# Performance work log

Hardware: AMD Instinct MI355X
Metric: run time of the kernel (lower is better)

The kernel has to match this reference:

```python
import jax, jax.numpy as jnp
import numpy as np

GROUP = 16  # FP4 quantization group size along the K (channel) axis
FP4_MAX = 6.0  # max magnitude representable in e2m1


def _round_e2m1(v):
    """Round to nearest value on the signed e2m1 grid {0,.5,1,1.5,2,3,4,6}."""
    s = jnp.sign(v)
    a = jnp.clip(jnp.abs(v), 0.0, FP4_MAX)
    q = jnp.where(a < 0.25, 0.0,
        jnp.where(a < 0.75, 0.5,
        jnp.where(a < 1.25, 1.0,
        jnp.where(a < 1.75, 1.5,
        jnp.where(a < 2.5, 2.0,
        jnp.where(a < 3.5, 3.0,
        jnp.where(a < 5.0, 4.0, 6.0)))))))
    return s * q


def fake_quant_fp4(x):
    """NVFP4-style fake quantization: per-16 group fp8_e4m3 scale + e2m1 values.

    x: [..., K] with K % 16 == 0. Returns dequantized tensor, same shape/dtype.
    """
    shp = x.shape
    g = x.reshape(shp[:-1] + (shp[-1] // GROUP, GROUP))
    amax = jnp.max(jnp.abs(g), axis=-1, keepdims=True)
    # scale stored as fp8_e4m3 (matches oscales dtype float8_e4m3fn in source)
    scale = (amax / FP4_MAX).astype(jnp.float8_e4m3fn).astype(x.dtype)
    safe = jnp.where(scale > 0, scale, jnp.ones_like(scale))
    q = _round_e2m1(g / safe)
    dq = jnp.where(scale > 0, q * scale, jnp.zeros_like(q))
    return dq.reshape(shp)


def setup_inputs() -> dict:
    key = jax.random.key(0)
    k1, k2, k3 = jax.random.split(key, 3)
    M, K, N = 8192, 4096, 4096
    x = jax.random.normal(k1, (M, K), dtype=jnp.float32)
    weight = jax.random.normal(k2, (N, K), dtype=jnp.float32) * 0.02
    bias = jax.random.normal(k3, (N,), dtype=jnp.float32) * 0.01
    return {"x": x, "weight": weight, "bias": bias}


def reference(x, weight, bias):
    # quantize_input: per-group FP4 fake-quant of activations (smooth == ones)
    xq = fake_quant_fp4(x)
    # __init__ quantizes weight_pad with the same kernel -> qweight/wscales
    wq = fake_quant_fp4(weight)
    # gemm_w4a4 with inline dequant + bias add
    out = jnp.einsum("mk,nk->mn", xq, wq) + bias
    return out
```

## Files before the change

kernel.cpp:

```cpp
#include <hip/hip_runtime.h>
#include <cstdint>


typedef __attribute__((ext_vector_type(8))) __bf16 bf16x8;
typedef __attribute__((ext_vector_type(4))) float f32x4;

typedef __attribute__((address_space(1))) void gvoid;
typedef __attribute__((address_space(3))) void lvoid;

__device__ __forceinline__ float fp8_e4m3_rt(float x) {
    if (x < 0.015625f) {
        return __builtin_rintf(x * 512.0f) * (1.0f / 512.0f);
    }
    unsigned u = __float_as_uint(x);
    unsigned lsb = (u >> 20) & 1u;
    u = (u + 0x7FFFFu + lsb) & ~0xFFFFFu;
    return __uint_as_float(u);
}

__device__ __forceinline__ float round_e2m1(float v) {
    float a = fabsf(v);
    a = fminf(a, 6.0f);
    float q = a < 0.25f ? 0.0f :
              a < 0.75f ? 0.5f :
              a < 1.25f ? 1.0f :
              a < 1.75f ? 1.5f :
              a < 2.5f  ? 2.0f :
              a < 3.5f  ? 3.0f :
              a < 5.0f  ? 4.0f : 6.0f;
    return copysignf(q, v);
}

__global__ __launch_bounds__(256) void quant_fp4(const float* __restrict__ in,
                                                 uint16_t* __restrict__ out,
                                                 int nquads) {
    int i = blockIdx.x * 256 + threadIdx.x;
    if (i >= nquads) return;
    float4 v = ((const float4*)in)[i];
    float a = fmaxf(fmaxf(fabsf(v.x), fabsf(v.y)), fmaxf(fabsf(v.z), fabsf(v.w)));
    a = fmaxf(a, __shfl_xor(a, 1));
    a = fmaxf(a, __shfl_xor(a, 2));
    float scale = fp8_e4m3_rt(a / 6.0f);
    float safe = scale > 0.0f ? scale : 1.0f;
    float vals[4] = {v.x, v.y, v.z, v.w};
    unsigned r[4];
    #pragma unroll
    for (int e = 0; e < 4; ++e) {
        float q = round_e2m1(vals[e] / safe);
        float dq = scale > 0.0f ? q * scale : 0.0f;
        r[e] = __float_as_uint(dq) >> 16;
    }
    uint2 o;
    o.x = r[0] | (r[1] << 16);
    o.y = r[2] | (r[3] << 16);
    ((uint2*)out)[i] = o;
}

#define BM 128
#define BN 128
#define BK 32

__global__ __launch_bounds__(256)
void gemm_w4a4(const uint16_t* __restrict__ Aq, const uint16_t* __restrict__ Bq,
               const float* __restrict__ bias, float* __restrict__ C,
               int M, int N, int K) {
    __shared__ __align__(16) uint16_t lA[BM * BK];
    __shared__ __align__(16) uint16_t lB[BN * BK];

    const int t    = threadIdx.x;
    const int wave = t >> 6;
    const int lane = t & 63;
    const int wm   = (wave >> 1) * 64;
    const int wn   = (wave & 1) * 64;
    const int mBase = blockIdx.y * BM;
    const int nBase = blockIdx.x * BN;
    const int lrow = lane & 15;
    const int kq   = (lane >> 4) * 8;

    f32x4 acc[4][4] = {};

    for (int k0 = 0; k0 < K; k0 += BK) {
        #pragma unroll
        for (int it = 0; it < 2; ++it) {
            const int c   = it * 256 + t;
            const int row = c >> 2;
            const int kc  = (c & 3) * 8;
            const uint16_t* gA = Aq + (size_t)(mBase + row) * K + (k0 + kc);
            const uint16_t* gB = Bq + (size_t)(nBase + row) * K + (k0 + kc);
            const int ldsOff = (it * 256 + wave * 64) * 8;
            __builtin_amdgcn_global_load_lds((gvoid*)gA, (lvoid*)&lA[ldsOff], 16, 0, 0);
            __builtin_amdgcn_global_load_lds((gvoid*)gB, (lvoid*)&lB[ldsOff], 16, 0, 0);
        }
        __syncthreads();

        bf16x8 af[4], bfr[4];
        #pragma unroll
        for (int i = 0; i < 4; ++i)
            af[i] = *(const bf16x8*)&lA[(wm + i * 16 + lrow) * BK + kq];
        #pragma unroll
        for (int j = 0; j < 4; ++j)
            bfr[j] = *(const bf16x8*)&lB[(wn + j * 16 + lrow) * BK + kq];

        #pragma unroll
        for (int i = 0; i < 4; ++i)
            #pragma unroll
            for (int j = 0; j < 4; ++j)
                acc[i][j] = __builtin_amdgcn_mfma_f32_16x16x32_bf16(
                    af[i], bfr[j], acc[i][j], 0, 0, 0);
        __syncthreads();
    }

    const int rq = (lane >> 4) * 4;
    #pragma unroll
    for (int j = 0; j < 4; ++j) {
        const int col = nBase + wn + j * 16 + lrow;
        const float bj = bias[col];
        #pragma unroll
        for (int i = 0; i < 4; ++i) {
            const int row0 = mBase + wm + i * 16 + rq;
            #pragma unroll
            for (int r = 0; r < 4; ++r)
                C[(size_t)(row0 + r) * N + col] = acc[i][j][r] + bj;
        }
    }
}

extern "C" void kernel_launch(void* const* d_in, const int* in_sizes, int n_in,
                              void* d_out, int out_size, void* d_ws, size_t ws_size,
                              hipStream_t stream) {
    const float* x    = (const float*)d_in[0];
    const float* w    = (const float*)d_in[1];
    const float* bias = (const float*)d_in[2];
    float* out = (float*)d_out;

    const int N = in_sizes[2];
    const int K = in_sizes[1] / N;
    const int M = in_sizes[0] / K;

    uint16_t* xq = (uint16_t*)d_ws;
    uint16_t* wq = xq + (size_t)M * K;

    const int xquads = (M * K) / 4;
    const int wquads = (N * K) / 4;
    quant_fp4<<<(xquads + 255) / 256, 256, 0, stream>>>(x, xq, xquads);
    quant_fp4<<<(wquads + 255) / 256, 256, 0, stream>>>(w, wq, wquads);

    dim3 grid(N / BN, M / BM);
    gemm_w4a4<<<grid, 256, 0, stream>>>(xq, wq, bias, out, M, N, K);
}
```

Measured before the change: 601.7 us.

## Rewrite bf16 GEMM with 256x256 tiles, double-buffered LDS and XCD remap

```diff
diff --git a/kernel.cpp b/kernel.cpp
--- a/kernel.cpp
+++ b/kernel.cpp
@@ -56,71 +56,164 @@
     ((uint2*)out)[i] = o;
 }
 
-#define BM 128
-#define BN 128
-#define BK 32
-
-__global__ __launch_bounds__(256)
+#define BM 256
+#define BN 256
+#define BK 64
+#define THREADS 512
+
+__device__ __forceinline__ void barfence() {
+    asm volatile("" ::: "memory");
+    __builtin_amdgcn_s_barrier();
+    asm volatile("" ::: "memory");
+}
+
+#define STG_A(bb, i, kk)                                                     \
+    __builtin_amdgcn_global_load_lds((gvoid*)(Aq + (size_t)offA[i] + (kk)),  \
+        (lvoid*)&lds[bb][0][ldsU + (i) * 4096], 16, 0, 0)
+#define STG_B(bb, i, kk)                                                     \
+    __builtin_amdgcn_global_load_lds((gvoid*)(Bq + (size_t)offB[i] + (kk)),  \
+        (lvoid*)&lds[bb][1][ldsU + (i) * 4096], 16, 0, 0)
+
+#define MFMA16(AH, BH, MH, NH)                                               \
+    _Pragma("unroll")                                                        \
+    for (int fi = 0; fi < 4; ++fi) {                                         \
+        _Pragma("unroll")                                                    \
+        for (int fj = 0; fj < 2; ++fj) {                                     \
+            f32x4 c = acc[(MH) * 4 + fi][(NH) * 2 + fj];                     \
+            c = __builtin_amdgcn_mfma_f32_16x16x32_bf16(AH[fi][0], BH[fj][0], c, 0, 0, 0); \
+            c = __builtin_amdgcn_mfma_f32_16x16x32_bf16(AH[fi][1], BH[fj][1], c, 0, 0, 0); \
+            acc[(MH) * 4 + fi][(NH) * 2 + fj] = c;                           \
+        }                                                                    \
+    }
+
+__global__ __launch_bounds__(THREADS, 2)
 void gemm_w4a4(const uint16_t* __restrict__ Aq, const uint16_t* __restrict__ Bq,
                const float* __restrict__ bias, float* __restrict__ C,
                int M, int N, int K) {
-    __shared__ __align__(16) uint16_t lA[BM * BK];
-    __shared__ __align__(16) uint16_t lB[BN * BK];
-
-    const int t    = threadIdx.x;
-    const int wave = t >> 6;
-    const int lane = t & 63;
-    const int wm   = (wave >> 1) * 64;
-    const int wn   = (wave & 1) * 64;
-    const int mBase = blockIdx.y * BM;
-    const int nBase = blockIdx.x * BN;
-    const int lrow = lane & 15;
-    const int kq   = (lane >> 4) * 8;
-
-    f32x4 acc[4][4] = {};
-
-    for (int k0 = 0; k0 < K; k0 += BK) {
-        #pragma unroll
-        for (int it = 0; it < 2; ++it) {
-            const int c   = it * 256 + t;
-            const int row = c >> 2;
-            const int kc  = (c & 3) * 8;
-            const uint16_t* gA = Aq + (size_t)(mBase + row) * K + (k0 + kc);
-            const uint16_t* gB = Bq + (size_t)(nBase + row) * K + (k0 + kc);
-            const int ldsOff = (it * 256 + wave * 64) * 8;
-            __builtin_amdgcn_global_load_lds((gvoid*)gA, (lvoid*)&lA[ldsOff], 16, 0, 0);
-            __builtin_amdgcn_global_load_lds((gvoid*)gB, (lvoid*)&lB[ldsOff], 16, 0, 0);
-        }
-        __syncthreads();
-
-        bf16x8 af[4], bfr[4];
-        #pragma unroll
-        for (int i = 0; i < 4; ++i)
-            af[i] = *(const bf16x8*)&lA[(wm + i * 16 + lrow) * BK + kq];
-        #pragma unroll
-        for (int j = 0; j < 4; ++j)
-            bfr[j] = *(const bf16x8*)&lB[(wn + j * 16 + lrow) * BK + kq];
-
-        #pragma unroll
-        for (int i = 0; i < 4; ++i)
+    __shared__ __align__(16) uint16_t lds[2][2][BM * BK];
+
+    const int tid  = threadIdx.x;
+    const int wave = tid >> 6;
+    const int lane = tid & 63;
+    const int wm   = wave >> 2;
+    const int wn   = wave & 3;
+    const int l15  = lane & 15;
+    const int l7   = lane & 7;
+    const int hi8  = (lane >> 4) << 3;
+    const int hi4  = (lane >> 4) << 2;
+    const int kx0  = hi8 ^ (l7 << 3);
+    const int kx1  = (32 + hi8) ^ (l7 << 3);
+    const int aBase = ((wm << 7) + l15) << 6;
+    const int bBase = ((wn << 6) + l15) << 6;
+    const int ldsU  = wave << 9;
+
+    const int ntm = M >> 8, ntn = N >> 8, nwg = ntm * ntn;
+    const int bid = blockIdx.x;
+    const int q8 = nwg >> 3, r8 = nwg & 7;
+    const int xcd = bid & 7;
+    const int wgid = (xcd < r8 ? xcd * (q8 + 1) : r8 * (q8 + 1) + (xcd - r8) * q8)
+                     + (bid >> 3);
+    const int mBase = (wgid % ntm) << 8;
+    const int nBase = (wgid / ntm) << 8;
+    (void)ntn;
+
+    uint32_t offA[4], offB[4];
+    #pragma unroll
+    for (int i = 0; i < 4; ++i) {
+        const int c   = i * THREADS + tid;
+        const int row = c >> 3;
+        const int kc  = ((c & 7) ^ (row & 7)) << 3;
+        offA[i] = (uint32_t)(mBase + row) * (uint32_t)K + (uint32_t)kc;
+        offB[i] = (uint32_t)(nBase + row) * (uint32_t)K + (uint32_t)kc;
+    }
+
+    const int nt = K / BK;
+
+    #pragma unroll
+    for (int i = 0; i < 4; ++i) STG_A(0, i, 0);
+    #pragma unroll
+    for (int i = 0; i < 4; ++i) STG_B(0, i, 0);
+    if (nt > 1) {
+        #pragma unroll
+        for (int i = 0; i < 4; ++i) STG_A(1, i, BK);
+        #pragma unroll
+        for (int i = 0; i < 4; ++i) STG_B(1, i, BK);
+    }
+
+    f32x4 acc[8][4] = {};
+
+    for (int tk = 0; tk < nt; ++tk) {
+        const int bb = tk & 1;
+        const uint16_t* lA = &lds[bb][0][0];
+        const uint16_t* lB = &lds[bb][1][0];
+        const int kk = (tk + 2) * BK;
+        const bool pf = (tk + 2) < nt;
+
+        if (tk + 1 < nt) { asm volatile("s_waitcnt vmcnt(8)" ::: "memory"); }
+        else             { asm volatile("s_waitcnt vmcnt(0)" ::: "memory"); }
+        __builtin_amdgcn_s_barrier();
+        asm volatile("" ::: "memory");
+
+        bf16x8 a[4][2], b0[2][2], b1[2][2];
+
+        #pragma unroll
+        for (int fi = 0; fi < 4; ++fi) {
+            a[fi][0] = *(const bf16x8*)&lA[aBase + fi * 1024 + kx0];
+            a[fi][1] = *(const bf16x8*)&lA[aBase + fi * 1024 + kx1];
+        }
+        #pragma unroll
+        for (int fj = 0; fj < 2; ++fj) {
+            b0[fj][0] = *(const bf16x8*)&lB[bBase + fj * 1024 + kx0];
+            b0[fj][1] = *(const bf16x8*)&lB[bBase + fj * 1024 + kx1];
+        }
+        barfence();
+        __builtin_amdgcn_s_setprio(1);
+        MFMA16(a, b0, 0, 0);
+        __builtin_amdgcn_s_setprio(0);
+        barfence();
+
+        #pragma unroll
+        for (int fj = 0; fj < 2; ++fj) {
+            b1[fj][0] = *(const bf16x8*)&lB[bBase + 2048 + fj * 1024 + kx0];
+            b1[fj][1] = *(const bf16x8*)&lB[bBase + 2048 + fj * 1024 + kx1];
+        }
+        if (pf) { STG_A(bb, 0, kk); STG_A(bb, 2, kk); }
+        barfence();
+        __builtin_amdgcn_s_setprio(1);
+        MFMA16(a, b1, 0, 1);
+        __builtin_amdgcn_s_setprio(0);
+        barfence();
+
+        #pragma unroll
+        for (int fi = 0; fi < 4; ++fi) {
+            a[fi][0] = *(const bf16x8*)&lA[aBase + 4096 + fi * 1024 + kx0];
+            a[fi][1] = *(const bf16x8*)&lA[aBase + 4096 + fi * 1024 + kx1];
+        }
+        if (pf) { STG_B(bb, 0, kk); STG_B(bb, 1, kk); }
+        barfence();
+        __builtin_amdgcn_s_setprio(1);
+        MFMA16(a, b1, 1, 1);
+        __builtin_amdgcn_s_setprio(0);
+        barfence();
+
+        if (pf) { STG_A(bb, 1, kk); STG_A(bb, 3, kk);
+                  STG_B(bb, 2, kk); STG_B(bb, 3, kk); }
+        barfence();
+        __builtin_amdgcn_s_setprio(1);
+        MFMA16(a, b0, 1, 0);
+        __builtin_amdgcn_s_setprio(0);
+    }
+
+    #pragma unroll
+    for (int fj = 0; fj < 4; ++fj) {
+        const int col = nBase + (wn << 6) + fj * 16 + l15;
+        const float bj = bias[col];
+        #pragma unroll
+        for (int fi = 0; fi < 8; ++fi) {
+            const int row0 = mBase + (wm << 7) + fi * 16 + hi4;
             #pragma unroll
-            for (int j = 0; j < 4; ++j)
-                acc[i][j] = __builtin_amdgcn_mfma_f32_16x16x32_bf16(
-                    af[i], bfr[j], acc[i][j], 0, 0, 0);
-        __syncthreads();
-    }
-
-    const int rq = (lane >> 4) * 4;
-    #pragma unroll
-    for (int j = 0; j < 4; ++j) {
-        const int col = nBase + wn + j * 16 + lrow;
-        const float bj = bias[col];
-        #pragma unroll
-        for (int i = 0; i < 4; ++i) {
-            const int row0 = mBase + wm + i * 16 + rq;
-            #pragma unroll
-            for (int r = 0; r < 4; ++r)
-                C[(size_t)(row0 + r) * N + col] = acc[i][j][r] + bj;
+            for (int rr = 0; rr < 4; ++rr)
+                C[(size_t)(row0 + rr) * N + col] = acc[fi][fj][rr] + bj;
         }
     }
 }
@@ -145,6 +238,6 @@
     quant_fp4<<<(xquads + 255) / 256, 256, 0, stream>>>(x, xq, xquads);
     quant_fp4<<<(wquads + 255) / 256, 256, 0, stream>>>(w, wq, wquads);
 
-    dim3 grid(N / BN, M / BM);
-    gemm_w4a4<<<grid, 256, 0, stream>>>(xq, wq, bias, out, M, N, K);
-}
+    const int nwg = (M >> 8) * (N >> 8);
+    gemm_w4a4<<<nwg, THREADS, 0, stream>>>(xq, wq, bias, out, M, N, K);
+}
```

Result: faster. 498.3 us (-17.2%).
